# Kernel tuning notes

Hardware: AMD Instinct MI355X
Metric: run time of the kernel (lower is better)

The kernel has to match this reference:

```python
import jax, jax.numpy as jnp
import numpy as np

N_NODES = 100000
N_EDGES = 1600000


def gcn_conv(x, src, dst, W, b, n_nodes):
    # GCNConv: linear transform, then symmetrically-normalized scatter-add
    # (self-loops already appended to src/dst by caller)
    h = x @ W  # [N, out]
    ones = jnp.ones(src.shape[0], dtype=x.dtype)
    deg = jax.ops.segment_sum(ones, dst, num_segments=n_nodes)  # in-degree incl. self-loop
    dinv = jnp.where(deg > 0, jax.lax.rsqrt(deg), jnp.zeros_like(deg))
    norm = dinv[src] * dinv[dst]  # [E]
    out = jax.ops.segment_sum(norm[:, None] * h[src], dst, num_segments=n_nodes)
    return out + b


def setup_inputs() -> dict:
    key = jax.random.key(0)
    ks = jax.random.split(key, 8)
    in_ch, nhid, out_ch = 128, 48, 32
    x = jax.random.normal(ks[0], (N_NODES, in_ch), dtype=jnp.float32)
    edge_index = jax.random.randint(ks[1], (2, N_EDGES), 0, N_NODES, dtype=jnp.int64)
    s1 = 1.0 / np.sqrt(in_ch)
    s2 = 1.0 / np.sqrt(nhid)
    W1 = jax.random.uniform(ks[2], (in_ch, nhid), jnp.float32, -s1, s1)
    b1 = jnp.zeros((nhid,), jnp.float32)
    Wmu = jax.random.uniform(ks[3], (nhid, out_ch), jnp.float32, -s2, s2)
    bmu = jnp.zeros((out_ch,), jnp.float32)
    Wls = jax.random.uniform(ks[4], (nhid, out_ch), jnp.float32, -s2, s2)
    bls = jnp.zeros((out_ch,), jnp.float32)
    return {"x": x, "edge_index": edge_index, "W1": W1, "b1": b1,
            "Wmu": Wmu, "bmu": bmu, "Wls": Wls, "bls": bls}


def reference(x, edge_index, W1, b1, Wmu, bmu, Wls, bls):
    n = x.shape[0]
    loop = jnp.arange(n, dtype=edge_index.dtype)
    src = jnp.concatenate([edge_index[0], loop])
    dst = jnp.concatenate([edge_index[1], loop])
    h = jax.nn.relu(gcn_conv(x, src, dst, W1, b1, n))
    mu = gcn_conv(h, src, dst, Wmu, bmu, n)
    logstd = gcn_conv(h, src, dst, Wls, bls, n)
    return mu, logstd
```

## Files before the change

### kernel.cpp

```cpp
#include <hip/hip_runtime.h>
#include <hip/hip_fp16.h>

#define NN 100000
#define NE 1600000
#define FIN 128
#define FH 48
#define FO 32
#define NODES_PER_BLOCK 21

#define LB 7
#define BKT_NODES 128
#define NBKT ((NN + BKT_NODES - 1) / BKT_NODES)
#define PBLK 250
#define EPB (NE / PBLK)
#define EPB4 (EPB / 4)
#define P2CAP 4096

__device__ inline float2 h2f2(unsigned int u) {
  __half2 h = __builtin_bit_cast(__half2, u);
  return __half22float2(h);
}
__device__ inline unsigned int f2h2(float a, float b) {
  __half2 h = __floats2half2_rn(a, b);
  return __builtin_bit_cast(unsigned int, h);
}


__global__ __launch_bounds__(256) void p1_hist(const int4* __restrict__ dst4, int* __restrict__ H) {
  __shared__ int hist[NBKT];
  const int t = threadIdx.x, blk = blockIdx.x;
  for (int i = t; i < NBKT; i += 256) hist[i] = 0;
  __syncthreads();
  const int k0 = blk * EPB4;
  for (int k = t; k < EPB4; k += 256) {
    int4 d = dst4[k0 + k];
    atomicAdd(&hist[d.x >> LB], 1);
    atomicAdd(&hist[d.y >> LB], 1);
    atomicAdd(&hist[d.z >> LB], 1);
    atomicAdd(&hist[d.w >> LB], 1);
  }
  __syncthreads();
  for (int i = t; i < NBKT; i += 256) H[blk * NBKT + i] = hist[i];
}

__global__ __launch_bounds__(256) void p1_colscan(int* __restrict__ H, int* __restrict__ tot) {
  int b = blockIdx.x * 256 + threadIdx.x;
  if (b >= NBKT) return;
  int run = 0;
  for (int xcd = 0; xcd < 8; ++xcd) {
    for (int blk = xcd; blk < PBLK; blk += 8) {
      int v = H[blk * NBKT + b];
      H[blk * NBKT + b] = run;
      run += v;
    }
  }
  tot[b] = run;
}

__global__ __launch_bounds__(256) void p1_scan(const int* __restrict__ tot, int* __restrict__ base,
                                               int* __restrict__ off) {
  __shared__ int s[256];
  const int t = threadIdx.x;
  int c[4]; int sum = 0;
  #pragma unroll
  for (int k = 0; k < 4; ++k) {
    int idx = 4 * t + k;
    c[k] = (idx < NBKT) ? tot[idx] : 0;
    sum += c[k];
  }
  s[t] = sum;
  __syncthreads();
  for (int o = 1; o < 256; o <<= 1) {
    int v = (t >= o) ? s[t - o] : 0;
    __syncthreads();
    s[t] += v;
    __syncthreads();
  }
  int run = s[t] - sum;
  #pragma unroll
  for (int k = 0; k < 4; ++k) {
    int idx = 4 * t + k;
    if (idx < NBKT) base[idx] = run;
    run += c[k];
  }
  if (t == 255) { base[NBKT] = run; off[NN] = run; }
}

__global__ __launch_bounds__(256) void p1_scatter(const int4* __restrict__ src4, const int4* __restrict__ dst4,
                                                  const int* __restrict__ H, const int* __restrict__ base,
                                                  int* __restrict__ pairs) {
  __shared__ int cur[NBKT];
  const int t = threadIdx.x, blk = blockIdx.x;
  for (int i = t; i < NBKT; i += 256) cur[i] = base[i] + H[blk * NBKT + i];
  __syncthreads();
  const int k0 = blk * EPB4;
  for (int k = t; k < EPB4; k += 256) {
    int4 s = src4[k0 + k];
    int4 d = dst4[k0 + k];
    int b0 = d.x >> LB, b1 = d.y >> LB, b2 = d.z >> LB, b3 = d.w >> LB;
    int p0 = atomicAdd(&cur[b0], 1);
    pairs[p0] = s.x | ((d.x & (BKT_NODES - 1)) << 17);
    int p1 = atomicAdd(&cur[b1], 1);
    pairs[p1] = s.y | ((d.y & (BKT_NODES - 1)) << 17);
    int p2 = atomicAdd(&cur[b2], 1);
    pairs[p2] = s.z | ((d.z & (BKT_NODES - 1)) << 17);
    int p3 = atomicAdd(&cur[b3], 1);
    pairs[p3] = s.w | ((d.w & (BKT_NODES - 1)) << 17);
  }
}

__global__ __launch_bounds__(256) void p2_bucket(const int* __restrict__ pairs, const int* __restrict__ base,
                                                 int* __restrict__ csr, int* __restrict__ off,
                                                 float* __restrict__ dinv) {
  __shared__ int stage[P2CAP];
  __shared__ int cnt[BKT_NODES];
  __shared__ int s[BKT_NODES];
  const int t = threadIdx.x, b = blockIdx.x;
  const int j0 = base[b], j1 = base[b + 1];
  const int ne = j1 - j0;
  const bool fits = (ne <= P2CAP);

  if (t < BKT_NODES) cnt[t] = 0;
  if (fits) {
    for (int j = t; j < ne; j += 256) stage[j] = pairs[j0 + j];
  }
  __syncthreads();
  if (fits) {
    for (int j = t; j < ne; j += 256) atomicAdd(&cnt[stage[j] >> 17], 1);
  } else {
    for (int j = j0 + t; j < j1; j += 256) atomicAdd(&cnt[pairs[j] >> 17], 1);
  }
  __syncthreads();
  int myc = 0;
  if (t < BKT_NODES) { myc = cnt[t]; s[t] = myc; }
  __syncthreads();
  for (int o = 1; o < BKT_NODES; o <<= 1) {
    int v = (t >= o && t < BKT_NODES) ? s[t - o] : 0;
    __syncthreads();
    if (t < BKT_NODES) s[t] += v;
    __syncthreads();
  }
  int loc = 0;
  if (t < BKT_NODES) loc = s[t] - myc;
  const int n = b * BKT_NODES + t;
  if (t < BKT_NODES && n < NN) {
    off[n] = j0 + loc;
    dinv[n] = rsqrtf((float)myc + 1.0f);
  }
  __syncthreads();
  if (t < BKT_NODES) s[t] = loc;
  __syncthreads();
  if (fits) {
    for (int j = t; j < ne; j += 256) {
      int p = stage[j];
      int pos = atomicAdd(&s[p >> 17], 1);
      csr[j0 + pos] = p & 0x1FFFF;
    }
  } else {
    for (int j = j0 + t; j < j1; j += 256) {
      int p = pairs[j];
      int pos = atomicAdd(&s[p >> 17], 1);
      csr[j0 + pos] = p & 0x1FFFF;
    }
  }
}


__global__ __launch_bounds__(256) void k_gemm1(const float* __restrict__ x, const float* __restrict__ W1,
                                               __half* __restrict__ t1h) {
  __shared__ float xs[64][132];
  __shared__ float ws[FIN][FH];
  const int t = threadIdx.x;
  const int row0 = blockIdx.x * 64;

  for (int i = t; i < FIN * FH; i += 256) ws[i / FH][i % FH] = W1[i];
  for (int i = t; i < 64 * (FIN / 4); i += 256) {
    int r = i >> 5, c4 = i & 31;
    float4 v = make_float4(0.f, 0.f, 0.f, 0.f);
    if (row0 + r < NN) v = ((const float4*)x)[(size_t)(row0 + r) * (FIN / 4) + c4];
    xs[r][c4 * 4 + 0] = v.x; xs[r][c4 * 4 + 1] = v.y;
    xs[r][c4 * 4 + 2] = v.z; xs[r][c4 * 4 + 3] = v.w;
  }
  __syncthreads();

  const int row = t >> 2;
  const int cg  = (t & 3) * 12;
  float acc[12];
  #pragma unroll
  for (int j = 0; j < 12; ++j) acc[j] = 0.f;

  #pragma unroll 4
  for (int k = 0; k < FIN; ++k) {
    float xv = xs[row][k];
    const float4* wp = (const float4*)&ws[k][cg];
    float4 w0 = wp[0], w1 = wp[1], w2 = wp[2];
    acc[0] += xv * w0.x; acc[1] += xv * w0.y; acc[2]  += xv * w0.z; acc[3]  += xv * w0.w;
    acc[4] += xv * w1.x; acc[5] += xv * w1.y; acc[6]  += xv * w1.z; acc[7]  += xv * w1.w;
    acc[8] += xv * w2.x; acc[9] += xv * w2.y; acc[10] += xv * w2.z; acc[11] += xv * w2.w;
  }

  const int grow = row0 + row;
  if (grow < NN) {
    uint2* p = (uint2*)(t1h + (size_t)grow * FH + cg);
    p[0] = make_uint2(f2h2(acc[0], acc[1]), f2h2(acc[2],  acc[3]));
    p[1] = make_uint2(f2h2(acc[4], acc[5]), f2h2(acc[6],  acc[7]));
    p[2] = make_uint2(f2h2(acc[8], acc[9]), f2h2(acc[10], acc[11]));
  }
}


__global__ __launch_bounds__(256) void k_gather1(const int* __restrict__ off, const int* __restrict__ csr,
                                                 const __half* __restrict__ feat16, const float* __restrict__ dinv,
                                                 const float* __restrict__ bias, __half* __restrict__ out16) {
  const int t = threadIdx.x;
  if (t >= NODES_PER_BLOCK * 12) return;
  const int local = t / 12;
  const int f4 = t - local * 12;
  const int node = blockIdx.x * NODES_PER_BLOCK + local;
  if (node >= NN) return;

  const uint2* feat8 = (const uint2*)feat16;
  const float di = dinv[node];
  const float sn = di * di;
  uint2 rs = feat8[(size_t)node * 12 + f4];
  float2 s01 = h2f2(rs.x), s23 = h2f2(rs.y);
  float4 acc = make_float4(s01.x * sn, s01.y * sn, s23.x * sn, s23.y * sn);

  int j = off[node];
  const int jend = off[node + 1];
  for (; j + 4 <= jend; j += 4) {
    int s0 = csr[j], s1 = csr[j + 1], s2 = csr[j + 2], s3 = csr[j + 3];
    float n0 = dinv[s0] * di, n1 = dinv[s1] * di, n2 = dinv[s2] * di, n3 = dinv[s3] * di;
    uint2 r0 = feat8[(size_t)s0 * 12 + f4];
    uint2 r1 = feat8[(size_t)s1 * 12 + f4];
    uint2 r2 = feat8[(size_t)s2 * 12 + f4];
    uint2 r3 = feat8[(size_t)s3 * 12 + f4];
    float2 a0 = h2f2(r0.x), b0 = h2f2(r0.y);
    float2 a1 = h2f2(r1.x), b1v = h2f2(r1.y);
    float2 a2 = h2f2(r2.x), b2 = h2f2(r2.y);
    float2 a3 = h2f2(r3.x), b3 = h2f2(r3.y);
    acc.x += n0 * a0.x; acc.y += n0 * a0.y; acc.z += n0 * b0.x; acc.w += n0 * b0.y;
    acc.x += n1 * a1.x; acc.y += n1 * a1.y; acc.z += n1 * b1v.x; acc.w += n1 * b1v.y;
    acc.x += n2 * a2.x; acc.y += n2 * a2.y; acc.z += n2 * b2.x; acc.w += n2 * b2.y;
    acc.x += n3 * a3.x; acc.y += n3 * a3.y; acc.z += n3 * b3.x; acc.w += n3 * b3.y;
  }
  for (; j < jend; ++j) {
    int s = csr[j];
    float nv = dinv[s] * di;
    uint2 r = feat8[(size_t)s * 12 + f4];
    float2 a = h2f2(r.x), b = h2f2(r.y);
    acc.x += nv * a.x; acc.y += nv * a.y; acc.z += nv * b.x; acc.w += nv * b.y;
  }

  const float4 bb = ((const float4*)bias)[f4];
  acc.x = fmaxf(acc.x + bb.x, 0.f);
  acc.y = fmaxf(acc.y + bb.y, 0.f);
  acc.z = fmaxf(acc.z + bb.z, 0.f);
  acc.w = fmaxf(acc.w + bb.w, 0.f);
  ((uint2*)out16)[(size_t)node * 12 + f4] = make_uint2(f2h2(acc.x, acc.y), f2h2(acc.z, acc.w));
}


__global__ __launch_bounds__(256) void k_gather_gemm2(const int* __restrict__ off, const int* __restrict__ csr,
                                                      const __half* __restrict__ feat16, const float* __restrict__ dinv,
                                                      const float* __restrict__ Wmu, const float* __restrict__ bmu,
                                                      const float* __restrict__ Wls, const float* __restrict__ bls,
                                                      float* __restrict__ out) {
  __shared__ float wall[FH][2 * FO];
  __shared__ float as2[NODES_PER_BLOCK][FH + 1];
  const int t = threadIdx.x;

  for (int i = t; i < FH * 2 * FO; i += 256) {
    int k = i >> 6, c = i & 63;
    wall[k][c] = (c < FO) ? Wmu[k * FO + c] : Wls[k * FO + (c - FO)];
  }

  const int local = t / 12;
  const int f4 = t - local * 12;
  const int node = blockIdx.x * NODES_PER_BLOCK + local;
  const bool active = (local < NODES_PER_BLOCK) && (node < NN);

  if (active) {
    const uint2* feat8 = (const uint2*)feat16;
    const float di = dinv[node];
    const float sn = di * di;
    uint2 rs = feat8[(size_t)node * 12 + f4];
    float2 s01 = h2f2(rs.x), s23 = h2f2(rs.y);
    float4 acc = make_float4(s01.x * sn, s01.y * sn, s23.x * sn, s23.y * sn);

    int j = off[node];
    const int jend = off[node + 1];
    for (; j + 4 <= jend; j += 4) {
      int s0 = csr[j], s1 = csr[j + 1], s2 = csr[j + 2], s3 = csr[j + 3];
      float n0 = dinv[s0] * di, n1 = dinv[s1] * di, n2 = dinv[s2] * di, n3 = dinv[s3] * di;
      uint2 r0 = feat8[(size_t)s0 * 12 + f4];
      uint2 r1 = feat8[(size_t)s1 * 12 + f4];
      uint2 r2 = feat8[(size_t)s2 * 12 + f4];
      uint2 r3 = feat8[(size_t)s3 * 12 + f4];
      float2 a0 = h2f2(r0.x), b0 = h2f2(r0.y);
      float2 a1 = h2f2(r1.x), b1v = h2f2(r1.y);
      float2 a2 = h2f2(r2.x), b2 = h2f2(r2.y);
      float2 a3 = h2f2(r3.x), b3 = h2f2(r3.y);
      acc.x += n0 * a0.x; acc.y += n0 * a0.y; acc.z += n0 * b0.x; acc.w += n0 * b0.y;
      acc.x += n1 * a1.x; acc.y += n1 * a1.y; acc.z += n1 * b1v.x; acc.w += n1 * b1v.y;
      acc.x += n2 * a2.x; acc.y += n2 * a2.y; acc.z += n2 * b2.x; acc.w += n2 * b2.y;
      acc.x += n3 * a3.x; acc.y += n3 * a3.y; acc.z += n3 * b3.x; acc.w += n3 * b3.y;
    }
    for (; j < jend; ++j) {
      int s = csr[j];
      float nv = dinv[s] * di;
      uint2 r = feat8[(size_t)s * 12 + f4];
      float2 a = h2f2(r.x), b = h2f2(r.y);
      acc.x += nv * a.x; acc.y += nv * a.y; acc.z += nv * b.x; acc.w += nv * b.y;
    }

    float* ap = &as2[local][f4 * 4];
    ap[0] = acc.x; ap[1] = acc.y; ap[2] = acc.z; ap[3] = acc.w;
  }
  __syncthreads();

  for (int o = t; o < NODES_PER_BLOCK * 2 * FO; o += 256) {
    const int ln = o >> 6;
    const int c = o & 63;
    const int grow = blockIdx.x * NODES_PER_BLOCK + ln;
    if (grow < NN) {
      float a = (c < FO) ? bmu[c] : bls[c - FO];
      #pragma unroll
      for (int k = 0; k < FH; ++k) a += as2[ln][k] * wall[k][c];
      if (c < FO) out[(size_t)grow * FO + c] = a;
      else        out[(size_t)NN * FO + (size_t)grow * FO + (c - FO)] = a;
    }
  }
}


extern "C" void kernel_launch(void* const* d_in, const int* in_sizes, int n_in,
                              void* d_out, int out_size, void* d_ws, size_t ws_size,
                              hipStream_t stream) {
  const float* x   = (const float*)d_in[0];
  const int*   ei  = (const int*)d_in[1];
  const float* W1  = (const float*)d_in[2];
  const float* b1  = (const float*)d_in[3];
  const float* Wmu = (const float*)d_in[4];
  const float* bmu = (const float*)d_in[5];
  const float* Wls = (const float*)d_in[6];
  const float* bls = (const float*)d_in[7];
  float* out = (float*)d_out;

  const int4* src4 = (const int4*)ei;
  const int4* dst4 = (const int4*)(ei + NE);

  char* base_p = (char*)d_ws;
  int*    pairs = (int*)base_p;
  int*    csr   = pairs + (size_t)NE;
  __half* t1h   = (__half*)(csr + (size_t)NE);
  __half* h16   = t1h + (size_t)NN * FH;
  int*    H     = (int*)(h16 + (size_t)NN * FH);
  int*    tot   = H + (size_t)PBLK * NBKT;
  int*    bkb   = tot + NBKT;
  int*    off   = bkb + NBKT + 1;
  float*  dinv  = (float*)(off + NN + 1);

  p1_hist   <<<PBLK, 256, 0, stream>>>(dst4, H);
  p1_colscan<<<(NBKT + 255) / 256, 256, 0, stream>>>(H, tot);
  p1_scan   <<<1, 256, 0, stream>>>(tot, bkb, off);
  p1_scatter<<<PBLK, 256, 0, stream>>>(src4, dst4, H, bkb, pairs);
  p2_bucket <<<NBKT, 256, 0, stream>>>(pairs, bkb, csr, off, dinv);

  k_gemm1<<<(NN + 63) / 64, 256, 0, stream>>>(x, W1, t1h);
  k_gather1<<<(NN + NODES_PER_BLOCK - 1) / NODES_PER_BLOCK, 256, 0, stream>>>(off, csr, t1h, dinv, b1, h16);

  k_gather_gemm2<<<(NN + NODES_PER_BLOCK - 1) / NODES_PER_BLOCK, 256, 0, stream>>>(
      off, csr, h16, dinv, Wmu, bmu, Wls, bls, out);
}
```

Baseline: 292.3 us.

## Stage block edge lists in LDS and widen gather loads to 16 bytes

Each gather block now processes 42 nodes, with 6 threads per node each loading uint4 (8 halves) instead of 12 threads loading uint2. The block's contiguous CSR segment and the matching dinv[src] values are first copied into shared memory, so the per-edge index and normalization loads come from LDS instead of dependent global reads. A fallback path handles blocks whose edge count exceeds the LDS capacity. The changes aim to cut global load instructions and dependent-load latency, at the cost of an extra barrier, more LDS per block and more registers per thread.

```diff
diff --git a/kernel.cpp b/kernel.cpp
--- a/kernel.cpp
+++ b/kernel.cpp
@@ -6,7 +6,6 @@
 #define FIN 128
 #define FH 48
 #define FO 32
-#define NODES_PER_BLOCK 21
 
 #define LB 7
 #define BKT_NODES 128
@@ -15,6 +14,9 @@
 #define EPB (NE / PBLK)
 #define EPB4 (EPB / 4)
 #define P2CAP 4096
+
+#define GNPB 42
+#define GCAP 1024
 
 __device__ inline float2 h2f2(unsigned int u) {
   __half2 h = __builtin_bit_cast(__half2, u);
@@ -209,55 +211,110 @@
 }
 
 
+#define GATHER_BODY(FEAT, SS, DS, A)                                             \
+  {                                                                              \
+    int j = jb;                                                                  \
+    for (; j + 4 <= je; j += 4) {                                                \
+      int s0 = SS[j], s1 = SS[j + 1], s2 = SS[j + 2], s3 = SS[j + 3];            \
+      float nv0 = DS[j] * di, nv1 = DS[j + 1] * di;                              \
+      float nv2 = DS[j + 2] * di, nv3 = DS[j + 3] * di;                          \
+      uint4 r0 = FEAT[(size_t)s0 * 6 + f8];                                      \
+      uint4 r1 = FEAT[(size_t)s1 * 6 + f8];                                      \
+      uint4 r2 = FEAT[(size_t)s2 * 6 + f8];                                      \
+      uint4 r3 = FEAT[(size_t)s3 * 6 + f8];                                      \
+      float2 q0, q1, q2, q3;                                                     \
+      q0 = h2f2(r0.x); q1 = h2f2(r0.y); q2 = h2f2(r0.z); q3 = h2f2(r0.w);        \
+      A[0] += nv0 * q0.x; A[1] += nv0 * q0.y; A[2] += nv0 * q1.x;                \
+      A[3] += nv0 * q1.y; A[4] += nv0 * q2.x; A[5] += nv0 * q2.y;                \
+      A[6] += nv0 * q3.x; A[7] += nv0 * q3.y;                                    \
+      q0 = h2f2(r1.x); q1 = h2f2(r1.y); q2 = h2f2(r1.z); q3 = h2f2(r1.w);        \
+      A[0] += nv1 * q0.x; A[1] += nv1 * q0.y; A[2] += nv1 * q1.x;                \
+      A[3] += nv1 * q1.y; A[4] += nv1 * q2.x; A[5] += nv1 * q2.y;                \
+      A[6] += nv1 * q3.x; A[7] += nv1 * q3.y;                                    \
+      q0 = h2f2(r2.x); q1 = h2f2(r2.y); q2 = h2f2(r2.z); q3 = h2f2(r2.w);        \
+      A[0] += nv2 * q0.x; A[1] += nv2 * q0.y; A[2] += nv2 * q1.x;                \
+      A[3] += nv2 * q1.y; A[4] += nv2 * q2.x; A[5] += nv2 * q2.y;                \
+      A[6] += nv2 * q3.x; A[7] += nv2 * q3.y;                                    \
+      q0 = h2f2(r3.x); q1 = h2f2(r3.y); q2 = h2f2(r3.z); q3 = h2f2(r3.w);        \
+      A[0] += nv3 * q0.x; A[1] += nv3 * q0.y; A[2] += nv3 * q1.x;                \
+      A[3] += nv3 * q1.y; A[4] += nv3 * q2.x; A[5] += nv3 * q2.y;                \
+      A[6] += nv3 * q3.x; A[7] += nv3 * q3.y;                                    \
+    }                                                                            \
+    for (; j < je; ++j) {                                                        \
+      int s = SS[j];                                                             \
+      float nv = DS[j] * di;                                                     \
+      uint4 r = FEAT[(size_t)s * 6 + f8];                                        \
+      float2 q0 = h2f2(r.x), q1 = h2f2(r.y), q2 = h2f2(r.z), q3 = h2f2(r.w);     \
+      A[0] += nv * q0.x; A[1] += nv * q0.y; A[2] += nv * q1.x;                   \
+      A[3] += nv * q1.y; A[4] += nv * q2.x; A[5] += nv * q2.y;                   \
+      A[6] += nv * q3.x; A[7] += nv * q3.y;                                      \
+    }                                                                            \
+  }
+
+
 __global__ __launch_bounds__(256) void k_gather1(const int* __restrict__ off, const int* __restrict__ csr,
                                                  const __half* __restrict__ feat16, const float* __restrict__ dinv,
                                                  const float* __restrict__ bias, __half* __restrict__ out16) {
+  __shared__ int   sstage[GCAP];
+  __shared__ float dstage[GCAP];
   const int t = threadIdx.x;
-  if (t >= NODES_PER_BLOCK * 12) return;
-  const int local = t / 12;
-  const int f4 = t - local * 12;
-  const int node = blockIdx.x * NODES_PER_BLOCK + local;
-  if (node >= NN) return;
-
-  const uint2* feat8 = (const uint2*)feat16;
+  const int n0 = blockIdx.x * GNPB;
+  const int nend = (n0 + GNPB < NN) ? n0 + GNPB : NN;
+  const int e0 = off[n0];
+  const int ec = off[nend] - e0;
+  const bool fits = (ec <= GCAP);
+  if (fits) {
+    for (int j = t; j < ec; j += 256) {
+      int s = csr[e0 + j];
+      sstage[j] = s;
+      dstage[j] = dinv[s];
+    }
+  }
+  __syncthreads();
+
+  const int local = t / 6;
+  const int f8 = t - local * 6;
+  const int node = n0 + local;
+  if (local >= GNPB || node >= NN) return;
+
+  const uint4* feat = (const uint4*)feat16;
   const float di = dinv[node];
   const float sn = di * di;
-  uint2 rs = feat8[(size_t)node * 12 + f4];
-  float2 s01 = h2f2(rs.x), s23 = h2f2(rs.y);
-  float4 acc = make_float4(s01.x * sn, s01.y * sn, s23.x * sn, s23.y * sn);
-
-  int j = off[node];
-  const int jend = off[node + 1];
-  for (; j + 4 <= jend; j += 4) {
-    int s0 = csr[j], s1 = csr[j + 1], s2 = csr[j + 2], s3 = csr[j + 3];
-    float n0 = dinv[s0] * di, n1 = dinv[s1] * di, n2 = dinv[s2] * di, n3 = dinv[s3] * di;
-    uint2 r0 = feat8[(size_t)s0 * 12 + f4];
-    uint2 r1 = feat8[(size_t)s1 * 12 + f4];
-    uint2 r2 = feat8[(size_t)s2 * 12 + f4];
-    uint2 r3 = feat8[(size_t)s3 * 12 + f4];
-    float2 a0 = h2f2(r0.x), b0 = h2f2(r0.y);
-    float2 a1 = h2f2(r1.x), b1v = h2f2(r1.y);
-    float2 a2 = h2f2(r2.x), b2 = h2f2(r2.y);
-    float2 a3 = h2f2(r3.x), b3 = h2f2(r3.y);
-    acc.x += n0 * a0.x; acc.y += n0 * a0.y; acc.z += n0 * b0.x; acc.w += n0 * b0.y;
-    acc.x += n1 * a1.x; acc.y += n1 * a1.y; acc.z += n1 * b1v.x; acc.w += n1 * b1v.y;
-    acc.x += n2 * a2.x; acc.y += n2 * a2.y; acc.z += n2 * b2.x; acc.w += n2 * b2.y;
-    acc.x += n3 * a3.x; acc.y += n3 * a3.y; acc.z += n3 * b3.x; acc.w += n3 * b3.y;
-  }
-  for (; j < jend; ++j) {
-    int s = csr[j];
-    float nv = dinv[s] * di;
-    uint2 r = feat8[(size_t)s * 12 + f4];
-    float2 a = h2f2(r.x), b = h2f2(r.y);
-    acc.x += nv * a.x; acc.y += nv * a.y; acc.z += nv * b.x; acc.w += nv * b.y;
-  }
-
-  const float4 bb = ((const float4*)bias)[f4];
-  acc.x = fmaxf(acc.x + bb.x, 0.f);
-  acc.y = fmaxf(acc.y + bb.y, 0.f);
-  acc.z = fmaxf(acc.z + bb.z, 0.f);
-  acc.w = fmaxf(acc.w + bb.w, 0.f);
-  ((uint2*)out16)[(size_t)node * 12 + f4] = make_uint2(f2h2(acc.x, acc.y), f2h2(acc.z, acc.w));
+  uint4 rs = feat[(size_t)node * 6 + f8];
+  float a[8];
+  {
+    float2 q0 = h2f2(rs.x), q1 = h2f2(rs.y), q2 = h2f2(rs.z), q3 = h2f2(rs.w);
+    a[0] = q0.x * sn; a[1] = q0.y * sn; a[2] = q1.x * sn; a[3] = q1.y * sn;
+    a[4] = q2.x * sn; a[5] = q2.y * sn; a[6] = q3.x * sn; a[7] = q3.y * sn;
+  }
+
+  if (fits) {
+    const int jb = off[node] - e0;
+    const int je = off[node + 1] - e0;
+    GATHER_BODY(feat, sstage, dstage, a)
+  } else {
+    const int jb = off[node];
+    const int je = off[node + 1];
+    for (int j = jb; j < je; ++j) {
+      int s = csr[j];
+      float nv = dinv[s] * di;
+      uint4 r = feat[(size_t)s * 6 + f8];
+      float2 q0 = h2f2(r.x), q1 = h2f2(r.y), q2 = h2f2(r.z), q3 = h2f2(r.w);
+      a[0] += nv * q0.x; a[1] += nv * q0.y; a[2] += nv * q1.x; a[3] += nv * q1.y;
+      a[4] += nv * q2.x; a[5] += nv * q2.y; a[6] += nv * q3.x; a[7] += nv * q3.y;
+    }
+  }
+
+  const float4* b4 = (const float4*)(bias + f8 * 8);
+  float4 bb0 = b4[0], bb1 = b4[1];
+  a[0] = fmaxf(a[0] + bb0.x, 0.f); a[1] = fmaxf(a[1] + bb0.y, 0.f);
+  a[2] = fmaxf(a[2] + bb0.z, 0.f); a[3] = fmaxf(a[3] + bb0.w, 0.f);
+  a[4] = fmaxf(a[4] + bb1.x, 0.f); a[5] = fmaxf(a[5] + bb1.y, 0.f);
+  a[6] = fmaxf(a[6] + bb1.z, 0.f); a[7] = fmaxf(a[7] + bb1.w, 0.f);
+  uint4 o;
+  o.x = f2h2(a[0], a[1]); o.y = f2h2(a[2], a[3]);
+  o.z = f2h2(a[4], a[5]); o.w = f2h2(a[6], a[7]);
+  ((uint4*)out16)[(size_t)node * 6 + f8] = o;
 }
 
 
@@ -266,69 +323,78 @@
                                                       const float* __restrict__ Wmu, const float* __restrict__ bmu,
                                                       const float* __restrict__ Wls, const float* __restrict__ bls,
                                                       float* __restrict__ out) {
+  __shared__ int   sstage[GCAP];
+  __shared__ float dstage[GCAP];
   __shared__ float wall[FH][2 * FO];
-  __shared__ float as2[NODES_PER_BLOCK][FH + 1];
+  __shared__ float as2[GNPB][FH + 1];
   const int t = threadIdx.x;
+  const int n0 = blockIdx.x * GNPB;
+  const int nend = (n0 + GNPB < NN) ? n0 + GNPB : NN;
+  const int e0 = off[n0];
+  const int ec = off[nend] - e0;
+  const bool fits = (ec <= GCAP);
 
   for (int i = t; i < FH * 2 * FO; i += 256) {
     int k = i >> 6, c = i & 63;
     wall[k][c] = (c < FO) ? Wmu[k * FO + c] : Wls[k * FO + (c - FO)];
   }
-
-  const int local = t / 12;
-  const int f4 = t - local * 12;
-  const int node = blockIdx.x * NODES_PER_BLOCK + local;
-  const bool active = (local < NODES_PER_BLOCK) && (node < NN);
+  if (fits) {
+    for (int j = t; j < ec; j += 256) {
+      int s = csr[e0 + j];
+      sstage[j] = s;
+      dstage[j] = dinv[s];
+    }
+  }
+  __syncthreads();
+
+  const int local = t / 6;
+  const int f8 = t - local * 6;
+  const int node = n0 + local;
+  const bool active = (local < GNPB) && (node < NN);
 
   if (active) {
-    const uint2* feat8 = (const uint2*)feat16;
+    const uint4* feat = (const uint4*)feat16;
     const float di = dinv[node];
     const float sn = di * di;
-    uint2 rs = feat8[(size_t)node * 12 + f4];
-    float2 s01 = h2f2(rs.x), s23 = h2f2(rs.y);
-    float4 acc = make_float4(s01.x * sn, s01.y * sn, s23.x * sn, s23.y * sn);
-
-    int j = off[node];
-    const int jend = off[node + 1];
-    for (; j + 4 <= jend; j += 4) {
-      int s0 = csr[j], s1 = csr[j + 1], s2 = csr[j + 2], s3 = csr[j + 3];
-      float n0 = dinv[s0] * di, n1 = dinv[s1] * di, n2 = dinv[s2] * di, n3 = dinv[s3] * di;
-      uint2 r0 = feat8[(size_t)s0 * 12 + f4];
-      uint2 r1 = feat8[(size_t)s1 * 12 + f4];
-      uint2 r2 = feat8[(size_t)s2 * 12 + f4];
-      uint2 r3 = feat8[(size_t)s3 * 12 + f4];
-      float2 a0 = h2f2(r0.x), b0 = h2f2(r0.y);
-      float2 a1 = h2f2(r1.x), b1v = h2f2(r1.y);
-      float2 a2 = h2f2(r2.x), b2 = h2f2(r2.y);
-      float2 a3 = h2f2(r3.x), b3 = h2f2(r3.y);
-      acc.x += n0 * a0.x; acc.y += n0 * a0.y; acc.z += n0 * b0.x; acc.w += n0 * b0.y;
-      acc.x += n1 * a1.x; acc.y += n1 * a1.y; acc.z += n1 * b1v.x; acc.w += n1 * b1v.y;
-      acc.x += n2 * a2.x; acc.y += n2 * a2.y; acc.z += n2 * b2.x; acc.w += n2 * b2.y;
-      acc.x += n3 * a3.x; acc.y += n3 * a3.y; acc.z += n3 * b3.x; acc.w += n3 * b3.y;
-    }
-    for (; j < jend; ++j) {
-      int s = csr[j];
-      float nv = dinv[s] * di;
-      uint2 r = feat8[(size_t)s * 12 + f4];
-      float2 a = h2f2(r.x), b = h2f2(r.y);
-      acc.x += nv * a.x; acc.y += nv * a.y; acc.z += nv * b.x; acc.w += nv * b.y;
-    }
-
-    float* ap = &as2[local][f4 * 4];
-    ap[0] = acc.x; ap[1] = acc.y; ap[2] = acc.z; ap[3] = acc.w;
-  }
-  __syncthreads();
-
-  for (int o = t; o < NODES_PER_BLOCK * 2 * FO; o += 256) {
+    uint4 rs = feat[(size_t)node * 6 + f8];
+    float a[8];
+    {
+      float2 q0 = h2f2(rs.x), q1 = h2f2(rs.y), q2 = h2f2(rs.z), q3 = h2f2(rs.w);
+      a[0] = q0.x * sn; a[1] = q0.y * sn; a[2] = q1.x * sn; a[3] = q1.y * sn;
+      a[4] = q2.x * sn; a[5] = q2.y * sn; a[6] = q3.x * sn; a[7] = q3.y * sn;
+    }
+    if (fits) {
+      const int jb = off[node] - e0;
+      const int je = off[node + 1] - e0;
+      GATHER_BODY(feat, sstage, dstage, a)
+    } else {
+      const int jb = off[node];
+      const int je = off[node + 1];
+      for (int j = jb; j < je; ++j) {
+        int s = csr[j];
+        float nv = dinv[s] * di;
+        uint4 r = feat[(size_t)s * 6 + f8];
+        float2 q0 = h2f2(r.x), q1 = h2f2(r.y), q2 = h2f2(r.z), q3 = h2f2(r.w);
+        a[0] += nv * q0.x; a[1] += nv * q0.y; a[2] += nv * q1.x; a[3] += nv * q1.y;
+        a[4] += nv * q2.x; a[5] += nv * q2.y; a[6] += nv * q3.x; a[7] += nv * q3.y;
+      }
+    }
+    float* ap = &as2[local][f8 * 8];
+    ap[0] = a[0]; ap[1] = a[1]; ap[2] = a[2]; ap[3] = a[3];
+    ap[4] = a[4]; ap[5] = a[5]; ap[6] = a[6]; ap[7] = a[7];
+  }
+  __syncthreads();
+
+  for (int o = t; o < GNPB * 2 * FO; o += 256) {
     const int ln = o >> 6;
     const int c = o & 63;
-    const int grow = blockIdx.x * NODES_PER_BLOCK + ln;
+    const int grow = n0 + ln;
     if (grow < NN) {
-      float a = (c < FO) ? bmu[c] : bls[c - FO];
+      float acc = (c < FO) ? bmu[c] : bls[c - FO];
       #pragma unroll
-      for (int k = 0; k < FH; ++k) a += as2[ln][k] * wall[k][c];
-      if (c < FO) out[(size_t)grow * FO + c] = a;
-      else        out[(size_t)NN * FO + (size_t)grow * FO + (c - FO)] = a;
+      for (int k = 0; k < FH; ++k) acc += as2[ln][k] * wall[k][c];
+      if (c < FO) out[(size_t)grow * FO + c] = acc;
+      else        out[(size_t)NN * FO + (size_t)grow * FO + (c - FO)] = acc;
     }
   }
 }
@@ -368,8 +434,8 @@
   p2_bucket <<<NBKT, 256, 0, stream>>>(pairs, bkb, csr, off, dinv);
 
   k_gemm1<<<(NN + 63) / 64, 256, 0, stream>>>(x, W1, t1h);
-  k_gather1<<<(NN + NODES_PER_BLOCK - 1) / NODES_PER_BLOCK, 256, 0, stream>>>(off, csr, t1h, dinv, b1, h16);
-
-  k_gather_gemm2<<<(NN + NODES_PER_BLOCK - 1) / NODES_PER_BLOCK, 256, 0, stream>>>(
+  k_gather1<<<(NN + GNPB - 1) / GNPB, 256, 0, stream>>>(off, csr, t1h, dinv, b1, h16);
+
+  k_gather_gemm2<<<(NN + GNPB - 1) / GNPB, 256, 0, stream>>>(
       off, csr, h16, dinv, Wmu, bmu, Wls, bls, out);
 }
```

Measured after the change: 292.7 us. About the same (+0.1%).
